# Performance work log

Measured on AMD Instinct MI355X. Metric: run time of the kernel, lower is better.

## Reference

```python
import jax, jax.numpy as jnp
import numpy as np


def setup_inputs() -> dict:
    key = jax.random.key(0)
    k1, k2, k3, k4, k5 = jax.random.split(key, 5)
    B, C, H, W = 4, 64, 64, 64
    Ck = C // 8
    x = jax.random.normal(k1, (B, C, H, W), dtype=jnp.float32)
    wq = jax.random.normal(k2, (Ck, C), dtype=jnp.float32) * (2.0 / C) ** 0.5
    wk = jax.random.normal(k3, (Ck, C), dtype=jnp.float32) * (2.0 / C) ** 0.5
    wv = jax.random.normal(k4, (C, C), dtype=jnp.float32) * (2.0 / C) ** 0.5
    gamma = jax.random.normal(k5, (1,), dtype=jnp.float32)
    return {"x": x, "wq": wq, "wk": wk, "wv": wv, "gamma": gamma}


def reference(x, wq, wk, wv, gamma):
    B, C, H, W = x.shape
    xf = x.reshape(B, C, H * W)                      # [B, C, N]
    f = jnp.einsum('kc,bcn->bkn', wq, xf)            # query: [B, C//8, N]
    g = jnp.einsum('kc,bcn->bkn', wk, xf)            # key:   [B, C//8, N]
    h = jnp.einsum('dc,bcn->bdn', wv, xf)            # value: [B, C, N]
    # f^T @ g -> [B, N, N]; NOTE: no 1/sqrt(d) scaling, softmax over dim=1 (rows)
    scores = jnp.einsum('bkn,bkm->bnm', f, g)
    beta = jax.nn.softmax(scores, axis=1)            # softmax over first N axis
    o = jnp.einsum('bcn,bnm->bcm', h, beta)          # h @ beta: [B, C, N]
    out = gamma[0] * o + xf
    return out.reshape(B, C, H, W)
```

## Files before the change

### kernel.cpp

```cpp
#include <hip/hip_runtime.h>
#include <hip/hip_bf16.h>
#include <cmath>

#define BATCH  4
#define CDIM   64
#define CK     8
#define NSEQ   4096
#define NSPLIT 8
#define NCHUNK (NSEQ / NSPLIT)
#define NSUBS  (NCHUNK / 32)
#define LOG2E  1.4426950408889634f

typedef __attribute__((ext_vector_type(8)))  short short8;
typedef __attribute__((ext_vector_type(16))) float f32x16;

__device__ inline unsigned short f2bf(float f) {
    union { float f; unsigned u; } v; v.f = f;
    unsigned r = v.u + 0x7fff + ((v.u >> 16) & 1);
    return (unsigned short)(r >> 16);
}
__device__ inline float bf2f(unsigned short h) {
    union { unsigned u; float f; } v; v.u = ((unsigned)h) << 16;
    return v.f;
}

__global__ __launch_bounds__(256) void prep_kernel(
    const float* __restrict__ x,  const float* __restrict__ wq,
    const float* __restrict__ wk, const float* __restrict__ wv,
    unsigned short* __restrict__ f_pair, unsigned short* __restrict__ g_pair,
    unsigned short* __restrict__ h_t)
{
    __shared__ __align__(16) float s_wq[CDIM][12];
    __shared__ __align__(16) float s_wk[CDIM][12];
    __shared__ __align__(16) unsigned short s_xt[4][32][72];

    const int t = threadIdx.x;

    if (blockIdx.x < 512) {
        #pragma unroll
        for (int u = 0; u < 2; ++u) {
            const int i = t + u * 256;
            const int k = i >> 6, c = i & 63;
            s_wq[c][k] = wq[i];
            s_wk[c][k] = wk[i];
        }
        __syncthreads();

        const int b  = blockIdx.x >> 7;
        const int n0 = (blockIdx.x & 127) * 32;
        const int nl = t >> 3;
        const int o  = t & 7;
        const int n  = n0 + nl;

        float fa[CK] = {0.f};
        float ga[CK] = {0.f};

        #pragma unroll
        for (int ci = 0; ci < 8; ++ci) {
            const int c   = 8 * o + ((ci + o) & 7);
            const float xv = x[(b * CDIM + c) * NSEQ + n];

            const float4 q0 = *(const float4*)&s_wq[c][0];
            const float4 q1 = *(const float4*)&s_wq[c][4];
            fa[0] += q0.x * xv; fa[1] += q0.y * xv; fa[2] += q0.z * xv; fa[3] += q0.w * xv;
            fa[4] += q1.x * xv; fa[5] += q1.y * xv; fa[6] += q1.z * xv; fa[7] += q1.w * xv;

            const float4 k0  = *(const float4*)&s_wk[c][0];
            const float4 k1v = *(const float4*)&s_wk[c][4];
            ga[0] += k0.x * xv; ga[1] += k0.y * xv; ga[2] += k0.z * xv; ga[3] += k0.w * xv;
            ga[4] += k1v.x * xv; ga[5] += k1v.y * xv; ga[6] += k1v.z * xv; ga[7] += k1v.w * xv;
        }

        #pragma unroll
        for (int k = 0; k < CK; ++k) {
            fa[k] += __shfl_xor(fa[k], 1); fa[k] += __shfl_xor(fa[k], 2); fa[k] += __shfl_xor(fa[k], 4);
            ga[k] += __shfl_xor(ga[k], 1); ga[k] += __shfl_xor(ga[k], 2); ga[k] += __shfl_xor(ga[k], 4);
        }

        if (o == 0) {
            unsigned short buf[16];
            #pragma unroll
            for (int k = 0; k < CK; ++k) {
                buf[k]     = f2bf(fa[k]);
                buf[8 + k] = f2bf(fa[k] - bf2f(buf[k]));
            }
            uint4* dst = (uint4*)&f_pair[(size_t)(b * NSEQ + n) * 16];
            dst[0] = ((const uint4*)buf)[0];
            dst[1] = ((const uint4*)buf)[1];
        }
        if (o == 1) {
            unsigned short buf[16];
            #pragma unroll
            for (int k = 0; k < CK; ++k) {
                const float gs = ga[k] * LOG2E;
                buf[k]     = f2bf(gs);
                buf[8 + k] = f2bf(gs - bf2f(buf[k]));
            }
            uint4* dst = (uint4*)&g_pair[(size_t)(b * NSEQ + n) * 16];
            dst[0] = ((const uint4*)buf)[0];
            dst[1] = ((const uint4*)buf)[1];
        }
    } else {
        const int w    = t >> 6;
        const int lane = t & 63;
        const int hh   = lane >> 5;
        const int lm   = lane & 31;

        const int tile = (blockIdx.x - 512) * 4 + w;
        const int b    = tile >> 7;
        const int n0   = (tile & 127) * 32;

        union U4 { short8 v; unsigned short us[8]; };
        U4 Avh[2][4], Avl[2][4];
        #pragma unroll
        for (int mt2 = 0; mt2 < 2; ++mt2) {
            const int row = mt2 * 32 + lm;
            #pragma unroll
            for (int kc = 0; kc < 4; ++kc) {
                const int k0 = kc * 16 + hh * 8;
                const float4 w0 = *(const float4*)&wv[row * 64 + k0];
                const float4 w1 = *(const float4*)&wv[row * 64 + k0 + 4];
                const float wf[8] = {w0.x, w0.y, w0.z, w0.w, w1.x, w1.y, w1.z, w1.w};
                #pragma unroll
                for (int j = 0; j < 8; ++j) {
                    const unsigned short hi = f2bf(wf[j]);
                    Avh[mt2][kc].us[j] = hi;
                    Avl[mt2][kc].us[j] = f2bf(wf[j] - bf2f(hi));
                }
            }
        }

        {
            const float* xs = &x[(size_t)(b * CDIM + lane) * NSEQ + n0];
            #pragma unroll
            for (int u = 0; u < 8; ++u) {
                const float4 v = *(const float4*)&xs[u * 4];
                s_xt[w][u*4 + 0][lane] = f2bf(v.x);
                s_xt[w][u*4 + 1][lane] = f2bf(v.y);
                s_xt[w][u*4 + 2][lane] = f2bf(v.z);
                s_xt[w][u*4 + 3][lane] = f2bf(v.w);
            }
        }
        __syncthreads();

        f32x16 acc0 = {}, acc1 = {};
        #pragma unroll
        for (int kc = 0; kc < 4; ++kc) {
            union U2x { short8 v; uint2 q[2]; } Bx;
            Bx.q[0] = *(const uint2*)&s_xt[w][lm][kc * 16 + hh * 8];
            Bx.q[1] = *(const uint2*)&s_xt[w][lm][kc * 16 + hh * 8 + 4];
            acc0 = __builtin_amdgcn_mfma_f32_32x32x16_bf16(Avh[0][kc].v, Bx.v, acc0, 0, 0, 0);
            acc0 = __builtin_amdgcn_mfma_f32_32x32x16_bf16(Avl[0][kc].v, Bx.v, acc0, 0, 0, 0);
            acc1 = __builtin_amdgcn_mfma_f32_32x32x16_bf16(Avh[1][kc].v, Bx.v, acc1, 0, 0, 0);
            acc1 = __builtin_amdgcn_mfma_f32_32x32x16_bf16(Avl[1][kc].v, Bx.v, acc1, 0, 0, 0);
        }

        __syncthreads();
        unsigned short* sh = &s_xt[w][0][0];
        const int nb_lo = lm >> 4, ne = lm & 15;
        #pragma unroll
        for (int r = 0; r < 16; ++r) {
            const int c0 = (r & 3) + 8 * (r >> 2) + 4 * hh;
            sh[(nb_lo * CDIM + c0)      * 16 + ne] = f2bf(acc0[r]);
            sh[(nb_lo * CDIM + 32 + c0) * 16 + ne] = f2bf(acc1[r]);
        }
        __syncthreads();
        uint4* dst = (uint4*)&h_t[(size_t)(b * (NSEQ / 16) + (n0 >> 4)) * (CDIM * 16)];
        const uint4* srcl = (const uint4*)sh;
        #pragma unroll
        for (int u = 0; u < 4; ++u)
            dst[u * 64 + lane] = srcl[u * 64 + lane];
    }
}

__global__ __launch_bounds__(512, 4) void attn_kernel(
    const unsigned short* __restrict__ f_pair,
    const unsigned short* __restrict__ g_pair,
    const unsigned short* __restrict__ h_t,
    const float* __restrict__ x, const float* __restrict__ gamma,
    float* __restrict__ out)
{
    __shared__ __align__(16) float s_o[CDIM][36];
    __shared__ __align__(16) float s_l[32];

    const int t    = threadIdx.x;
    const int w    = t >> 6;
    const int lane = t & 63;
    const int hh   = lane >> 5;
    const int lm   = lane & 31;

    const int bid = blockIdx.x;
    const int mt  = bid & 127;
    const int b   = bid >> 7;
    const int s   = w;

    const int m = mt * 32 + lm;

    union U4 { short8 v; uint4 q4; unsigned u[4]; unsigned short us[8]; };

    U4 Bgh, Bgl;
    {
        const uint4* gp = (const uint4*)&g_pair[(size_t)(b * NSEQ + m) * 16];
        Bgh.q4 = gp[0];
        Bgl.q4 = gp[1];
    }

    f32x16 acc0 = {}, acc1 = {};
    float lsA = 0.f, lsB = 0.f;

    const unsigned short* fp = f_pair + (size_t)b * NSEQ * 16
                             + (size_t)lm * 16 + hh * 8;
    const unsigned short* ht = h_t + (size_t)(b * (NSEQ / 16) + s * (NCHUNK / 16)) * (CDIM * 16)
                             + hh * 8;

    auto loadAf = [&](int j) -> short8 {
        return *(const short8*)&fp[(size_t)(s * NCHUNK + j * 32) * 16];
    };
    auto loadH = [&](int j, uint4 (&ha)[2], uint4 (&hb2)[2]) {
        #pragma unroll
        for (int ks = 0; ks < 2; ++ks) {
            ha[ks]  = *(const uint4*)&ht[(size_t)((j * 2 + ks) * CDIM + lm) * 16];
            hb2[ks] = *(const uint4*)&ht[(size_t)((j * 2 + ks) * CDIM + 32 + lm) * 16];
        }
    };

    short8 af[2];
    uint4  hA[2][2], hB[2][2];

    af[0] = loadAf(0); loadH(0, hA[0], hB[0]);
    af[1] = loadAf(1); loadH(1, hA[1], hB[1]);

    #pragma unroll
    for (int j = 0; j < NSUBS; ++j) {
        const int cur = j & 1;

        const f32x16 kZ = {};
        f32x16 sc = __builtin_amdgcn_mfma_f32_32x32x16_bf16(af[cur], Bgh.v, kZ, 0, 0, 0);
        sc = __builtin_amdgcn_mfma_f32_32x32x16_bf16(af[cur], Bgl.v, sc, 0, 0, 0);

        if (j + 2 < NSUBS) af[cur] = loadAf(j + 2);

        unsigned a[8];
        #pragma unroll
        for (int p = 0; p < 8; ++p) {
            const float e0 = __builtin_amdgcn_exp2f(sc[2*p]);
            const float e1 = __builtin_amdgcn_exp2f(sc[2*p+1]);
            lsA += e0; lsB += e1;
            __hip_bfloat162 h2 = __float22bfloat162_rn(make_float2(e0, e1));
            a[p] = *(unsigned*)&h2;
        }
        const auto s02 = __builtin_amdgcn_permlane32_swap(a[0], a[2], false, false);
        const auto s13 = __builtin_amdgcn_permlane32_swap(a[1], a[3], false, false);
        const auto s46 = __builtin_amdgcn_permlane32_swap(a[4], a[6], false, false);
        const auto s57 = __builtin_amdgcn_permlane32_swap(a[5], a[7], false, false);

        U4 P0, P1;
        P0.u[0] = s02[0]; P0.u[1] = s13[0]; P0.u[2] = s02[1]; P0.u[3] = s13[1];
        P1.u[0] = s46[0]; P1.u[1] = s57[0]; P1.u[2] = s46[1]; P1.u[3] = s57[1];

        union U2x { short8 v; uint4 q; } Ax;
        __builtin_amdgcn_s_setprio(1);
        Ax.q = hA[cur][0];
        acc0 = __builtin_amdgcn_mfma_f32_32x32x16_bf16(Ax.v, P0.v, acc0, 0, 0, 0);
        Ax.q = hB[cur][0];
        acc1 = __builtin_amdgcn_mfma_f32_32x32x16_bf16(Ax.v, P0.v, acc1, 0, 0, 0);
        Ax.q = hA[cur][1];
        acc0 = __builtin_amdgcn_mfma_f32_32x32x16_bf16(Ax.v, P1.v, acc0, 0, 0, 0);
        Ax.q = hB[cur][1];
        acc1 = __builtin_amdgcn_mfma_f32_32x32x16_bf16(Ax.v, P1.v, acc1, 0, 0, 0);
        __builtin_amdgcn_s_setprio(0);

        if (j + 2 < NSUBS) loadH(j + 2, hA[cur], hB[cur]);
    }

    const float lsum = lsA + lsB;
    const float ltot = lsum + __shfl_xor(lsum, 32);

    #pragma unroll
    for (int ws = 0; ws < NSPLIT; ++ws) {
        if (w == ws) {
            if (ws == 0) {
                #pragma unroll
                for (int r = 0; r < 16; ++r) {
                    const int c0 = (r & 3) + 8 * (r >> 2) + 4 * hh;
                    s_o[c0][lm]      = acc0[r];
                    s_o[32 + c0][lm] = acc1[r];
                }
                if (hh == 0) s_l[lm] = ltot;
            } else {
                #pragma unroll
                for (int r = 0; r < 16; ++r) {
                    const int c0 = (r & 3) + 8 * (r >> 2) + 4 * hh;
                    s_o[c0][lm]      += acc0[r];
                    s_o[32 + c0][lm] += acc1[r];
                }
                if (hh == 0) s_l[lm] += ltot;
            }
        }
        __syncthreads();
    }

    {
        const float g  = gamma[0];
        const int   c  = t >> 3;
        const int   mg = (t & 7) * 4;
        const float4 ov = *(const float4*)&s_o[c][mg];
        const float4 lv = *(const float4*)&s_l[mg];
        const size_t idx = (size_t)(b * CDIM + c) * NSEQ + mt * 32 + mg;
        const float4 xv = *(const float4*)&x[idx];
        float4 r;
        r.x = g * ov.x / lv.x + xv.x;
        r.y = g * ov.y / lv.y + xv.y;
        r.z = g * ov.z / lv.z + xv.z;
        r.w = g * ov.w / lv.w + xv.w;
        *(float4*)&out[idx] = r;
    }
}

extern "C" void kernel_launch(void* const* d_in, const int* in_sizes, int n_in,
                              void* d_out, int out_size, void* d_ws, size_t ws_size,
                              hipStream_t stream) {
    const float* x     = (const float*)d_in[0];
    const float* wq    = (const float*)d_in[1];
    const float* wk    = (const float*)d_in[2];
    const float* wv    = (const float*)d_in[3];
    const float* gamma = (const float*)d_in[4];
    float* out = (float*)d_out;

    char* wsb = (char*)d_ws;
    unsigned short* f_pair = (unsigned short*)wsb;
    unsigned short* g_pair = f_pair + (size_t)BATCH * NSEQ * 16;
    unsigned short* h_t    = g_pair + (size_t)BATCH * NSEQ * 16;

    hipLaunchKernelGGL(prep_kernel, dim3(640), dim3(256), 0, stream,
                       x, wq, wk, wv, f_pair, g_pair, h_t);
    hipLaunchKernelGGL(attn_kernel, dim3(BATCH * 128), dim3(512), 0, stream,
                       f_pair, g_pair, h_t, x, gamma, out);
}
```

Measured before the change: 36.05 us.

## Process 64 query columns per block to reuse F and H tiles across two column tiles

Each attention block now handles 64 output columns (two 32-wide tiles) instead of 32. Every loaded f and h fragment feeds twice as many MFMAs, which halves global/L2 traffic per unit of work. The grid drops to 256 blocks, batch becomes the low bits of the block index, and occupancy bounds are lowered to 2 for the larger register footprint. The serialized per-wave LDS reduction with eight barriers is replaced by LDS atomicAdd into a zeroed buffer. The risks are fewer blocks than the 256 CUs can fully exploit for latency hiding, and higher register pressure.

```diff
diff --git a/kernel.cpp b/kernel.cpp
--- a/kernel.cpp
+++ b/kernel.cpp
@@ -173,15 +173,15 @@
     }
 }
 
-__global__ __launch_bounds__(512, 4) void attn_kernel(
+__global__ __launch_bounds__(512, 2) void attn_kernel(
     const unsigned short* __restrict__ f_pair,
     const unsigned short* __restrict__ g_pair,
     const unsigned short* __restrict__ h_t,
     const float* __restrict__ x, const float* __restrict__ gamma,
     float* __restrict__ out)
 {
-    __shared__ __align__(16) float s_o[CDIM][36];
-    __shared__ __align__(16) float s_l[32];
+    __shared__ __align__(16) float s_o[CDIM][68];
+    __shared__ __align__(16) float s_l[CDIM];
 
     const int t    = threadIdx.x;
     const int w    = t >> 6;
@@ -190,23 +190,36 @@
     const int lm   = lane & 31;
 
     const int bid = blockIdx.x;
-    const int mt  = bid & 127;
-    const int b   = bid >> 7;
+    const int b   = bid & 3;
+    const int mt  = bid >> 2;
     const int s   = w;
 
-    const int m = mt * 32 + lm;
+    const int m0 = mt * 64 + lm;
+    const int m1 = m0 + 32;
+
+    {
+        float* sz = &s_o[0][0];
+        #pragma unroll
+        for (int u = 0; u < 9; ++u) {
+            const int i = t + u * 512;
+            if (i < CDIM * 68) sz[i] = 0.f;
+        }
+        if (t < CDIM) s_l[t] = 0.f;
+    }
+    __syncthreads();
 
     union U4 { short8 v; uint4 q4; unsigned u[4]; unsigned short us[8]; };
 
-    U4 Bgh, Bgl;
+    U4 Bgh0, Bgl0, Bgh1, Bgl1;
     {
-        const uint4* gp = (const uint4*)&g_pair[(size_t)(b * NSEQ + m) * 16];
-        Bgh.q4 = gp[0];
-        Bgl.q4 = gp[1];
-    }
-
-    f32x16 acc0 = {}, acc1 = {};
-    float lsA = 0.f, lsB = 0.f;
+        const uint4* gp0 = (const uint4*)&g_pair[(size_t)(b * NSEQ + m0) * 16];
+        Bgh0.q4 = gp0[0];  Bgl0.q4 = gp0[1];
+        const uint4* gp1 = (const uint4*)&g_pair[(size_t)(b * NSEQ + m1) * 16];
+        Bgh1.q4 = gp1[0];  Bgl1.q4 = gp1[1];
+    }
+
+    f32x16 acc0 = {}, acc1 = {}, acc2 = {}, acc3 = {};
+    float ls0A = 0.f, ls0B = 0.f, ls1A = 0.f, ls1B = 0.f;
 
     const unsigned short* fp = f_pair + (size_t)b * NSEQ * 16
                              + (size_t)lm * 16 + hh * 8;
@@ -223,29 +236,13 @@
             hb2[ks] = *(const uint4*)&ht[(size_t)((j * 2 + ks) * CDIM + 32 + lm) * 16];
         }
     };
-
-    short8 af[2];
-    uint4  hA[2][2], hB[2][2];
-
-    af[0] = loadAf(0); loadH(0, hA[0], hB[0]);
-    af[1] = loadAf(1); loadH(1, hA[1], hB[1]);
-
-    #pragma unroll
-    for (int j = 0; j < NSUBS; ++j) {
-        const int cur = j & 1;
-
-        const f32x16 kZ = {};
-        f32x16 sc = __builtin_amdgcn_mfma_f32_32x32x16_bf16(af[cur], Bgh.v, kZ, 0, 0, 0);
-        sc = __builtin_amdgcn_mfma_f32_32x32x16_bf16(af[cur], Bgl.v, sc, 0, 0, 0);
-
-        if (j + 2 < NSUBS) af[cur] = loadAf(j + 2);
-
+    auto mkP = [&](const f32x16& sc, U4& Pk0, U4& Pk1, float& lA, float& lB) {
         unsigned a[8];
         #pragma unroll
         for (int p = 0; p < 8; ++p) {
             const float e0 = __builtin_amdgcn_exp2f(sc[2*p]);
             const float e1 = __builtin_amdgcn_exp2f(sc[2*p+1]);
-            lsA += e0; lsB += e1;
+            lA += e0; lB += e1;
             __hip_bfloat162 h2 = __float22bfloat162_rn(make_float2(e0, e1));
             a[p] = *(unsigned*)&h2;
         }
@@ -253,67 +250,88 @@
         const auto s13 = __builtin_amdgcn_permlane32_swap(a[1], a[3], false, false);
         const auto s46 = __builtin_amdgcn_permlane32_swap(a[4], a[6], false, false);
         const auto s57 = __builtin_amdgcn_permlane32_swap(a[5], a[7], false, false);
-
-        U4 P0, P1;
-        P0.u[0] = s02[0]; P0.u[1] = s13[0]; P0.u[2] = s02[1]; P0.u[3] = s13[1];
-        P1.u[0] = s46[0]; P1.u[1] = s57[0]; P1.u[2] = s46[1]; P1.u[3] = s57[1];
+        Pk0.u[0] = s02[0]; Pk0.u[1] = s13[0]; Pk0.u[2] = s02[1]; Pk0.u[3] = s13[1];
+        Pk1.u[0] = s46[0]; Pk1.u[1] = s57[0]; Pk1.u[2] = s46[1]; Pk1.u[3] = s57[1];
+    };
+
+    short8 af[2];
+    uint4  hA[2][2], hB[2][2];
+
+    af[0] = loadAf(0); loadH(0, hA[0], hB[0]);
+    af[1] = loadAf(1); loadH(1, hA[1], hB[1]);
+
+    #pragma unroll
+    for (int j = 0; j < NSUBS; ++j) {
+        const int cur = j & 1;
+
+        const f32x16 kZ = {};
+        f32x16 sc0 = __builtin_amdgcn_mfma_f32_32x32x16_bf16(af[cur], Bgh0.v, kZ, 0, 0, 0);
+        sc0 = __builtin_amdgcn_mfma_f32_32x32x16_bf16(af[cur], Bgl0.v, sc0, 0, 0, 0);
+        f32x16 sc1 = __builtin_amdgcn_mfma_f32_32x32x16_bf16(af[cur], Bgh1.v, kZ, 0, 0, 0);
+        sc1 = __builtin_amdgcn_mfma_f32_32x32x16_bf16(af[cur], Bgl1.v, sc1, 0, 0, 0);
+
+        if (j + 2 < NSUBS) af[cur] = loadAf(j + 2);
+
+        U4 P00, P01, P10, P11;
+        mkP(sc0, P00, P01, ls0A, ls0B);
+        mkP(sc1, P10, P11, ls1A, ls1B);
 
         union U2x { short8 v; uint4 q; } Ax;
         __builtin_amdgcn_s_setprio(1);
         Ax.q = hA[cur][0];
-        acc0 = __builtin_amdgcn_mfma_f32_32x32x16_bf16(Ax.v, P0.v, acc0, 0, 0, 0);
+        acc0 = __builtin_amdgcn_mfma_f32_32x32x16_bf16(Ax.v, P00.v, acc0, 0, 0, 0);
+        acc2 = __builtin_amdgcn_mfma_f32_32x32x16_bf16(Ax.v, P10.v, acc2, 0, 0, 0);
         Ax.q = hB[cur][0];
-        acc1 = __builtin_amdgcn_mfma_f32_32x32x16_bf16(Ax.v, P0.v, acc1, 0, 0, 0);
+        acc1 = __builtin_amdgcn_mfma_f32_32x32x16_bf16(Ax.v, P00.v, acc1, 0, 0, 0);
+        acc3 = __builtin_amdgcn_mfma_f32_32x32x16_bf16(Ax.v, P10.v, acc3, 0, 0, 0);
         Ax.q = hA[cur][1];
-        acc0 = __builtin_amdgcn_mfma_f32_32x32x16_bf16(Ax.v, P1.v, acc0, 0, 0, 0);
+        acc0 = __builtin_amdgcn_mfma_f32_32x32x16_bf16(Ax.v, P01.v, acc0, 0, 0, 0);
+        acc2 = __builtin_amdgcn_mfma_f32_32x32x16_bf16(Ax.v, P11.v, acc2, 0, 0, 0);
         Ax.q = hB[cur][1];
-        acc1 = __builtin_amdgcn_mfma_f32_32x32x16_bf16(Ax.v, P1.v, acc1, 0, 0, 0);
+        acc1 = __builtin_amdgcn_mfma_f32_32x32x16_bf16(Ax.v, P01.v, acc1, 0, 0, 0);
+        acc3 = __builtin_amdgcn_mfma_f32_32x32x16_bf16(Ax.v, P11.v, acc3, 0, 0, 0);
         __builtin_amdgcn_s_setprio(0);
 
         if (j + 2 < NSUBS) loadH(j + 2, hA[cur], hB[cur]);
     }
 
-    const float lsum = lsA + lsB;
-    const float ltot = lsum + __shfl_xor(lsum, 32);
-
-    #pragma unroll
-    for (int ws = 0; ws < NSPLIT; ++ws) {
-        if (w == ws) {
-            if (ws == 0) {
-                #pragma unroll
-                for (int r = 0; r < 16; ++r) {
-                    const int c0 = (r & 3) + 8 * (r >> 2) + 4 * hh;
-                    s_o[c0][lm]      = acc0[r];
-                    s_o[32 + c0][lm] = acc1[r];
-                }
-                if (hh == 0) s_l[lm] = ltot;
-            } else {
-                #pragma unroll
-                for (int r = 0; r < 16; ++r) {
-                    const int c0 = (r & 3) + 8 * (r >> 2) + 4 * hh;
-                    s_o[c0][lm]      += acc0[r];
-                    s_o[32 + c0][lm] += acc1[r];
-                }
-                if (hh == 0) s_l[lm] += ltot;
-            }
-        }
-        __syncthreads();
-    }
+    {
+        const float l0 = ls0A + ls0B;
+        const float l1 = ls1A + ls1B;
+        const float lt0 = l0 + __shfl_xor(l0, 32);
+        const float lt1 = l1 + __shfl_xor(l1, 32);
+        if (hh == 0) {
+            atomicAdd(&s_l[lm], lt0);
+            atomicAdd(&s_l[32 + lm], lt1);
+        }
+        #pragma unroll
+        for (int r = 0; r < 16; ++r) {
+            const int c0 = (r & 3) + 8 * (r >> 2) + 4 * hh;
+            atomicAdd(&s_o[c0][lm],           acc0[r]);
+            atomicAdd(&s_o[32 + c0][lm],      acc1[r]);
+            atomicAdd(&s_o[c0][32 + lm],      acc2[r]);
+            atomicAdd(&s_o[32 + c0][32 + lm], acc3[r]);
+        }
+    }
+    __syncthreads();
 
     {
         const float g  = gamma[0];
         const int   c  = t >> 3;
-        const int   mg = (t & 7) * 4;
-        const float4 ov = *(const float4*)&s_o[c][mg];
-        const float4 lv = *(const float4*)&s_l[mg];
-        const size_t idx = (size_t)(b * CDIM + c) * NSEQ + mt * 32 + mg;
-        const float4 xv = *(const float4*)&x[idx];
-        float4 r;
-        r.x = g * ov.x / lv.x + xv.x;
-        r.y = g * ov.y / lv.y + xv.y;
-        r.z = g * ov.z / lv.z + xv.z;
-        r.w = g * ov.w / lv.w + xv.w;
-        *(float4*)&out[idx] = r;
+        const int   mg = (t & 7) * 8;
+        const size_t idx = (size_t)(b * CDIM + c) * NSEQ + mt * 64 + mg;
+        #pragma unroll
+        for (int h = 0; h < 2; ++h) {
+            const float4 ov = *(const float4*)&s_o[c][mg + h * 4];
+            const float4 lv = *(const float4*)&s_l[mg + h * 4];
+            const float4 xv = *(const float4*)&x[idx + h * 4];
+            float4 r;
+            r.x = g * ov.x / lv.x + xv.x;
+            r.y = g * ov.y / lv.y + xv.y;
+            r.z = g * ov.z / lv.z + xv.z;
+            r.w = g * ov.w / lv.w + xv.w;
+            *(float4*)&out[idx + h * 4] = r;
+        }
     }
 }
 
@@ -334,6 +352,6 @@
 
     hipLaunchKernelGGL(prep_kernel, dim3(640), dim3(256), 0, stream,
                        x, wq, wk, wv, f_pair, g_pair, h_t);
-    hipLaunchKernelGGL(attn_kernel, dim3(BATCH * 128), dim3(512), 0, stream,
+    hipLaunchKernelGGL(attn_kernel, dim3(BATCH * 64), dim3(512), 0, stream,
                        f_pair, g_pair, h_t, x, gamma, out);
 }
```

After: 67.54 us. 87.4% more time.
